# Kernel tuning notes

Hardware: AMD Instinct MI355X
Metric: run time of the kernel (lower is better)

The kernel has to match this reference:

```python
import jax, jax.numpy as jnp
import numpy as np

N = 1_000_000
MU_PRIOR = 0.6447


def setup_inputs() -> dict:
    key = jax.random.key(0)
    ks = jax.random.split(key, 8)
    pred_ = jax.random.normal(ks[0], (N, 9), jnp.float32)
    Y_obs = jax.random.normal(ks[1], (N, 9), jnp.float32)
    rrs = jax.random.normal(ks[2], (N, 5), jnp.float32)
    rrs_pred = jax.random.normal(ks[3], (N, 5), jnp.float32)
    nan_array = jax.random.normal(ks[4], (N, 9), jnp.float32)  # all finite -> lens = 9
    # cov_z must be SPD so log(det(cov_z)) is finite
    A = jax.random.normal(ks[5], (N, 3, 3), jnp.float32) * 0.3
    cov_z = jnp.einsum('nij,nkj->nik', A, A) + 0.5 * jnp.eye(3, dtype=jnp.float32)
    mu_z = jax.random.normal(ks[6], (N, 3), jnp.float32)
    parameters = 1.0 + 0.01 * jax.random.normal(ks[7], (64,), jnp.float32)
    return {"pred_": pred_, "Y_obs": Y_obs, "rrs": rrs, "rrs_pred": rrs_pred,
            "nan_array": nan_array, "cov_z": cov_z, "mu_z": mu_z,
            "parameters": parameters}


def reference(pred_, Y_obs, rrs, rrs_pred, nan_array, cov_z, mu_z, parameters):
    n = pred_.shape[0]
    # --- buffers built in __init__ (default multipliers = ones) ---
    se_diag = jnp.asarray([0.0015, 0.0012, 0.001, 0.00086, 0.00057], jnp.float32) ** 2
    rrs_cov_inv = jnp.linalg.inv(jnp.diag(se_diag))            # [5,5]
    Y_cov_inv = jnp.eye(9, dtype=jnp.float32)                  # [9,9]
    s_a = jnp.eye(3, dtype=jnp.float32) * 4.9                  # [3,3]
    s_a_inv = jnp.linalg.inv(s_a)                              # [3,3]

    # trace((X) @ Cinv @ X.T) == sum_n x_n^T Cinv x_n  (trace trick, O(N))
    dr = rrs - rrs_pred                                        # [N,5]
    rrs_error = jnp.einsum('ni,ij,nj->', dr, rrs_cov_inv, dr) / (5.0 * n)

    lens = jnp.sum(~jnp.isnan(nan_array), axis=1).astype(jnp.float32)  # [N]
    dy = pred_ - Y_obs                                         # [N,9]
    obs_quad = jnp.einsum('ni,ij,nj->n', dy, Y_cov_inv, dy)    # [N]
    obs_error = jnp.sum(obs_quad / lens) / n

    # KL(N(mu_z, cov_z) || N(0.6447, s_a)) style term
    logdet_sa = jnp.log(jnp.linalg.det(s_a))
    logdet_cz = jnp.log(jnp.linalg.det(cov_z))                 # [N]
    tr_term = jnp.einsum('ij,nji->n', s_a_inv, cov_z)          # trace(s_a_inv @ cov_z)
    dm = mu_z - MU_PRIOR                                       # [N,3]
    DK = 0.5 * jnp.sum(logdet_sa - logdet_cz + tr_term) / n \
         + 0.5 * jnp.einsum('ni,ij,nj->', dm, s_a_inv, dm) / (3.0 * n)

    l2_norm = jnp.mean((parameters - 1.0) ** 2)
    return rrs_error + 10.0 * obs_error + DK + l2_norm
```

## Files before the change

### kernel.cpp

```cpp
#include <hip/hip_runtime.h>
#include <math.h>

#define MU_PRIOR   0.6447f
#define LOGDET_SA  4.767705615349743f
#define INV_SA     (1.0f/4.9f)

#define CW      64
#define NF4C    144
#define NF4R    80
#define NF4M    48
#define GRID    2048

#define W0 (1.0f / (0.0015f  * 0.0015f))
#define W1 (1.0f / (0.0012f  * 0.0012f))
#define W2 (1.0f / (0.0010f  * 0.0010f))
#define W3 (1.0f / (0.00086f * 0.00086f))
#define W4 (1.0f / (0.00057f * 0.00057f))

__device__ __forceinline__ float warp_reduce_f(float v) {
#pragma unroll
    for (int off = 32; off > 0; off >>= 1) v += __shfl_down(v, off, 64);
    return v;
}

__device__ __forceinline__ double warp_reduce_d(double v) {
#pragma unroll
    for (int off = 32; off > 0; off >>= 1) v += __shfl_down(v, off, 64);
    return v;
}

__device__ __forceinline__ float comb1(float p, float y, float n) {
    const float d = p - y;
    const float d2 = d * d;
    const unsigned u = __float_as_uint(d2) | ((n == n) ? 0u : 0x80000000u);
    return __uint_as_float(u);
}
__device__ __forceinline__ float4 comb4(float4 p, float4 y, float4 n) {
    float4 o;
    o.x = comb1(p.x, y.x, n.x); o.y = comb1(p.y, y.y, n.y);
    o.z = comb1(p.z, y.z, n.z); o.w = comb1(p.w, y.w, n.w);
    return o;
}

__global__ __launch_bounds__(256) void loss_main(
    const float* __restrict__ pred, const float* __restrict__ yobs,
    const float* __restrict__ rrs,  const float* __restrict__ rrsp,
    const float* __restrict__ nanarr, const float* __restrict__ cov,
    const float* __restrict__ mu, double* __restrict__ partial, int nchunks)
{
    __shared__ float4 sV[4 * NF4C];
    __shared__ float4 sC[4 * NF4C];

    const int tid  = threadIdx.x;
    const int lane = tid & 63;
    const int wid  = tid >> 6;
    const int wslot = wid * NF4C;
    const int wgid  = blockIdx.x * 4 + wid;
    const int nw    = (int)gridDim.x * 4;

    const int w0 = (5 - (lane % 5)) % 5;
    float ew[5];
#pragma unroll
    for (int k = 0; k < 5; ++k) {
        int idx = w0 + k; if (idx >= 5) idx -= 5;
        ew[k] = (idx == 0) ? W0 : (idx == 1) ? W1 : (idx == 2) ? W2
               : (idx == 3) ? W3 : W4;
    }

    float acc = 0.0f;

    for (int c = wgid; c < nchunks; c += nw) {
        const float4* gP = reinterpret_cast<const float4*>(pred)   + (size_t)c * NF4C;
        const float4* gY = reinterpret_cast<const float4*>(yobs)   + (size_t)c * NF4C;
        const float4* gN = reinterpret_cast<const float4*>(nanarr) + (size_t)c * NF4C;
        const float4* gC = reinterpret_cast<const float4*>(cov)    + (size_t)c * NF4C;
        const float4* gR = reinterpret_cast<const float4*>(rrs)    + (size_t)c * NF4R;
        const float4* gQ = reinterpret_cast<const float4*>(rrsp)   + (size_t)c * NF4R;
        const float4* gM = reinterpret_cast<const float4*>(mu)     + (size_t)c * NF4M;

        const float4 p0 = gP[lane], p1 = gP[lane + 64];
        const float4 y0 = gY[lane], y1 = gY[lane + 64];
        const float4 n0 = gN[lane], n1 = gN[lane + 64];
        const float4 c0 = gC[lane], c1 = gC[lane + 64];
        const float4 r0 = gR[lane], q0 = gQ[lane];
        float4 p2, y2, n2, c2, r1, q1, m0;
        if (lane < 16) {
            p2 = gP[lane + 128]; y2 = gY[lane + 128];
            n2 = gN[lane + 128]; c2 = gC[lane + 128];
            r1 = gR[lane + 64];  q1 = gQ[lane + 64];
        }
        if (lane < 48) m0 = gM[lane];

        {
            float ra = 0.f;
            const float d0 = r0.x - q0.x, d1 = r0.y - q0.y;
            const float d2 = r0.z - q0.z, d3 = r0.w - q0.w;
            ra += d0 * d0 * ew[0] + d1 * d1 * ew[1]
                + d2 * d2 * ew[2] + d3 * d3 * ew[3];
            if (lane < 16) {
                const float e0 = r1.x - q1.x, e1 = r1.y - q1.y;
                const float e2 = r1.z - q1.z, e3 = r1.w - q1.w;
                ra += e0 * e0 * ew[1] + e1 * e1 * ew[2]
                    + e2 * e2 * ew[3] + e3 * e3 * ew[4];
            }
            acc += ra * 0.2f;
        }

        if (lane < 48) {
            const float d0 = m0.x - MU_PRIOR, d1 = m0.y - MU_PRIOR;
            const float d2 = m0.z - MU_PRIOR, d3 = m0.w - MU_PRIOR;
            acc += (d0 * d0 + d1 * d1 + d2 * d2 + d3 * d3) * (1.0f / 29.4f);
        }

        sV[wslot + lane]       = comb4(p0, y0, n0);
        sV[wslot + lane + 64]  = comb4(p1, y1, n1);
        sC[wslot + lane]       = c0;
        sC[wslot + lane + 64]  = c1;
        if (lane < 16) {
            sV[wslot + lane + 128] = comb4(p2, y2, n2);
            sC[wslot + lane + 128] = c2;
        }

        __builtin_amdgcn_wave_barrier();

        {
            const float* v = reinterpret_cast<const float*>(sV + wslot) + 9 * lane;
            const float* m = reinterpret_cast<const float*>(sC + wslot) + 9 * lane;
            float dy2 = 0.f, len = 0.f;
#pragma unroll
            for (int k = 0; k < 9; ++k) {
                const unsigned u = __float_as_uint(v[k]);
                dy2 += __uint_as_float(u & 0x7fffffffu);
                len += (float)(1u - (u >> 31));
            }
            acc += 10.0f * dy2 / len;

            const float tr  = m[0] + m[4] + m[8];
            const float det = m[0] * (m[4] * m[8] - m[5] * m[7])
                            - m[1] * (m[3] * m[8] - m[5] * m[6])
                            + m[2] * (m[3] * m[7] - m[4] * m[6]);
            acc += 0.5f * (LOGDET_SA - __logf(det) + tr * INV_SA);
        }

        __builtin_amdgcn_wave_barrier();
    }

    acc = warp_reduce_f(acc);
    __shared__ float smem[4];
    if (lane == 0) smem[wid] = acc;
    __syncthreads();
    if (tid == 0)
        partial[blockIdx.x] = (double)(smem[0] + smem[1] + smem[2] + smem[3]);
}

__global__ __launch_bounds__(256) void loss_final(
    const double* __restrict__ partial, int npartials,
    const float* __restrict__ params, int nparams,
    const float* __restrict__ pred, const float* __restrict__ yobs,
    const float* __restrict__ rrs,  const float* __restrict__ rrsp,
    const float* __restrict__ nanarr, const float* __restrict__ cov,
    const float* __restrict__ mu, int mainRows, int rows,
    float* __restrict__ out)
{
    double accA = 0.0;
    double accB = 0.0;

    for (int i = threadIdx.x; i < npartials; i += 256) accA += partial[i];
    for (int i = threadIdx.x; i < nparams; i += 256) {
        const float d = params[i] - 1.0f;
        accB += (double)(d * d);
    }

    for (int r = mainRows + (int)threadIdx.x; r < rows; r += 256) {
        float dy2 = 0.f, len = 0.f;
        for (int i = 0; i < 9; ++i) {
            const float d = pred[9 * (size_t)r + i] - yobs[9 * (size_t)r + i];
            dy2 += d * d;
            const float v = nanarr[9 * (size_t)r + i];
            len += (v == v) ? 1.f : 0.f;
        }
        const float W[5] = {W0, W1, W2, W3, W4};
        float racc = 0.f;
        for (int i = 0; i < 5; ++i) {
            const float d = rrs[5 * (size_t)r + i] - rrsp[5 * (size_t)r + i];
            racc += d * d * W[i];
        }
        const float* m = cov + 9 * (size_t)r;
        const float tr  = m[0] + m[4] + m[8];
        const float det = m[0] * (m[4] * m[8] - m[5] * m[7])
                        - m[1] * (m[3] * m[8] - m[5] * m[6])
                        + m[2] * (m[3] * m[7] - m[4] * m[6]);
        float dm = 0.f;
        for (int i = 0; i < 3; ++i) {
            const float d = mu[3 * (size_t)r + i] - MU_PRIOR;
            dm += d * d;
        }
        accA += (double)(racc * 0.2f + 10.f * dy2 / len
                         + 0.5f * (LOGDET_SA - __logf(det) + tr * INV_SA)
                         + dm * (1.f / 29.4f));
    }

    double val = accA * (1.0 / (double)rows) + accB * (1.0 / (double)nparams);
    val = warp_reduce_d(val);
    __shared__ double sm[4];
    const int lane = threadIdx.x & 63;
    const int wid  = threadIdx.x >> 6;
    if (lane == 0) sm[wid] = val;
    __syncthreads();
    if (threadIdx.x == 0)
        out[0] = (float)(sm[0] + sm[1] + sm[2] + sm[3]);
}

extern "C" void kernel_launch(void* const* d_in, const int* in_sizes, int n_in,
                              void* d_out, int out_size, void* d_ws, size_t ws_size,
                              hipStream_t stream) {
    const float* pred   = (const float*)d_in[0];
    const float* yobs   = (const float*)d_in[1];
    const float* rrs    = (const float*)d_in[2];
    const float* rrsp   = (const float*)d_in[3];
    const float* nanarr = (const float*)d_in[4];
    const float* cov    = (const float*)d_in[5];
    const float* mu     = (const float*)d_in[6];
    const float* params = (const float*)d_in[7];
    float* out = (float*)d_out;

    const int rows     = in_sizes[0] / 9;
    const int nchunks  = rows / CW;
    const int mainRows = nchunks * CW;
    int grid = (nchunks * 4 < GRID * 4) ? ((nchunks + 3) / 4 > 0 ? (nchunks + 3) / 4 : 1) : GRID;
    if (grid > GRID) grid = GRID;

    double* partial = (double*)d_ws;

    loss_main<<<grid, 256, 0, stream>>>(pred, yobs, rrs, rrsp, nanarr,
                                        cov, mu, partial, nchunks);
    loss_final<<<1, 256, 0, stream>>>(partial, grid, params, in_sizes[7],
                                      pred, yobs, rrs, rrsp, nanarr, cov, mu,
                                      mainRows, rows, out);
}
```

Before: 208.1 us.

## Fuse final reduction into main kernel and double-buffer chunk loads per wave

The separate final-reduction kernel is replaced by a last-block-done pattern, using an atomic counter reset by a memset before launch. Each wave now issues global loads for two chunks before computing either, to raise memory-level parallelism. The grid is sized so each wave handles pairs of chunks. This costs higher register pressure, which could lower occupancy, plus an extra memset operation and atomic traffic.

```diff
diff --git a/kernel.cpp b/kernel.cpp
--- a/kernel.cpp
+++ b/kernel.cpp
@@ -42,18 +42,117 @@
     return o;
 }
 
-__global__ __launch_bounds__(256) void loss_main(
+struct ChunkRegs {
+    float4 p0, p1, p2, y0, y1, y2, n0, n1, n2, c0, c1, c2;
+    float4 r0, q0, r1, q1, m0;
+};
+
+__device__ __forceinline__ void issue_loads(
+    ChunkRegs& R, int c, int lane,
     const float* __restrict__ pred, const float* __restrict__ yobs,
     const float* __restrict__ rrs,  const float* __restrict__ rrsp,
     const float* __restrict__ nanarr, const float* __restrict__ cov,
-    const float* __restrict__ mu, double* __restrict__ partial, int nchunks)
+    const float* __restrict__ mu)
+{
+    const float4* gP = reinterpret_cast<const float4*>(pred)   + (size_t)c * NF4C;
+    const float4* gY = reinterpret_cast<const float4*>(yobs)   + (size_t)c * NF4C;
+    const float4* gN = reinterpret_cast<const float4*>(nanarr) + (size_t)c * NF4C;
+    const float4* gC = reinterpret_cast<const float4*>(cov)    + (size_t)c * NF4C;
+    const float4* gR = reinterpret_cast<const float4*>(rrs)    + (size_t)c * NF4R;
+    const float4* gQ = reinterpret_cast<const float4*>(rrsp)   + (size_t)c * NF4R;
+    const float4* gM = reinterpret_cast<const float4*>(mu)     + (size_t)c * NF4M;
+
+    R.p0 = gP[lane]; R.p1 = gP[lane + 64];
+    R.y0 = gY[lane]; R.y1 = gY[lane + 64];
+    R.n0 = gN[lane]; R.n1 = gN[lane + 64];
+    R.c0 = gC[lane]; R.c1 = gC[lane + 64];
+    R.r0 = gR[lane]; R.q0 = gQ[lane];
+    if (lane < 16) {
+        R.p2 = gP[lane + 128]; R.y2 = gY[lane + 128];
+        R.n2 = gN[lane + 128]; R.c2 = gC[lane + 128];
+        R.r1 = gR[lane + 64];  R.q1 = gQ[lane + 64];
+    }
+    if (lane < 48) R.m0 = gM[lane];
+}
+
+__device__ __forceinline__ float compute_chunk(
+    const ChunkRegs& R, float4* __restrict__ sVw, float4* __restrict__ sCw,
+    int lane, const float ew[5])
+{
+    float acc = 0.0f;
+
+    {
+        float ra = 0.f;
+        const float d0 = R.r0.x - R.q0.x, d1 = R.r0.y - R.q0.y;
+        const float d2 = R.r0.z - R.q0.z, d3 = R.r0.w - R.q0.w;
+        ra += d0 * d0 * ew[0] + d1 * d1 * ew[1]
+            + d2 * d2 * ew[2] + d3 * d3 * ew[3];
+        if (lane < 16) {
+            const float e0 = R.r1.x - R.q1.x, e1 = R.r1.y - R.q1.y;
+            const float e2 = R.r1.z - R.q1.z, e3 = R.r1.w - R.q1.w;
+            ra += e0 * e0 * ew[1] + e1 * e1 * ew[2]
+                + e2 * e2 * ew[3] + e3 * e3 * ew[4];
+        }
+        acc += ra * 0.2f;
+    }
+
+    if (lane < 48) {
+        const float d0 = R.m0.x - MU_PRIOR, d1 = R.m0.y - MU_PRIOR;
+        const float d2 = R.m0.z - MU_PRIOR, d3 = R.m0.w - MU_PRIOR;
+        acc += (d0 * d0 + d1 * d1 + d2 * d2 + d3 * d3) * (1.0f / 29.4f);
+    }
+
+    sVw[lane]       = comb4(R.p0, R.y0, R.n0);
+    sVw[lane + 64]  = comb4(R.p1, R.y1, R.n1);
+    sCw[lane]       = R.c0;
+    sCw[lane + 64]  = R.c1;
+    if (lane < 16) {
+        sVw[lane + 128] = comb4(R.p2, R.y2, R.n2);
+        sCw[lane + 128] = R.c2;
+    }
+
+    __builtin_amdgcn_wave_barrier();
+
+    {
+        const float* v = reinterpret_cast<const float*>(sVw) + 9 * lane;
+        const float* m = reinterpret_cast<const float*>(sCw) + 9 * lane;
+        float dy2 = 0.f, len = 0.f;
+#pragma unroll
+        for (int k = 0; k < 9; ++k) {
+            const unsigned u = __float_as_uint(v[k]);
+            dy2 += __uint_as_float(u & 0x7fffffffu);
+            len += (float)(1u - (u >> 31));
+        }
+        acc += 10.0f * dy2 / len;
+
+        const float tr  = m[0] + m[4] + m[8];
+        const float det = m[0] * (m[4] * m[8] - m[5] * m[7])
+                        - m[1] * (m[3] * m[8] - m[5] * m[6])
+                        + m[2] * (m[3] * m[7] - m[4] * m[6]);
+        acc += 0.5f * (LOGDET_SA - __logf(det) + tr * INV_SA);
+    }
+
+    __builtin_amdgcn_wave_barrier();
+    return acc;
+}
+
+__global__ __launch_bounds__(256) void loss_fused(
+    const float* __restrict__ pred, const float* __restrict__ yobs,
+    const float* __restrict__ rrs,  const float* __restrict__ rrsp,
+    const float* __restrict__ nanarr, const float* __restrict__ cov,
+    const float* __restrict__ mu, const float* __restrict__ params,
+    double* __restrict__ partial, unsigned* __restrict__ counter,
+    int nchunks, int rows, int nparams, float* __restrict__ out)
 {
     __shared__ float4 sV[4 * NF4C];
     __shared__ float4 sC[4 * NF4C];
-
-    const int tid  = threadIdx.x;
-    const int lane = tid & 63;
-    const int wid  = tid >> 6;
+    __shared__ float  smem[4];
+    __shared__ double smd[4];
+    __shared__ int    amLast;
+
+    const int tid   = threadIdx.x;
+    const int lane  = tid & 63;
+    const int wid   = tid >> 6;
     const int wslot = wid * NF4C;
     const int wgid  = blockIdx.x * 4 + wid;
     const int nw    = (int)gridDim.x * 4;
@@ -69,109 +168,45 @@
 
     float acc = 0.0f;
 
-    for (int c = wgid; c < nchunks; c += nw) {
-        const float4* gP = reinterpret_cast<const float4*>(pred)   + (size_t)c * NF4C;
-        const float4* gY = reinterpret_cast<const float4*>(yobs)   + (size_t)c * NF4C;
-        const float4* gN = reinterpret_cast<const float4*>(nanarr) + (size_t)c * NF4C;
-        const float4* gC = reinterpret_cast<const float4*>(cov)    + (size_t)c * NF4C;
-        const float4* gR = reinterpret_cast<const float4*>(rrs)    + (size_t)c * NF4R;
-        const float4* gQ = reinterpret_cast<const float4*>(rrsp)   + (size_t)c * NF4R;
-        const float4* gM = reinterpret_cast<const float4*>(mu)     + (size_t)c * NF4M;
-
-        const float4 p0 = gP[lane], p1 = gP[lane + 64];
-        const float4 y0 = gY[lane], y1 = gY[lane + 64];
-        const float4 n0 = gN[lane], n1 = gN[lane + 64];
-        const float4 c0 = gC[lane], c1 = gC[lane + 64];
-        const float4 r0 = gR[lane], q0 = gQ[lane];
-        float4 p2, y2, n2, c2, r1, q1, m0;
-        if (lane < 16) {
-            p2 = gP[lane + 128]; y2 = gY[lane + 128];
-            n2 = gN[lane + 128]; c2 = gC[lane + 128];
-            r1 = gR[lane + 64];  q1 = gQ[lane + 64];
-        }
-        if (lane < 48) m0 = gM[lane];
-
-        {
-            float ra = 0.f;
-            const float d0 = r0.x - q0.x, d1 = r0.y - q0.y;
-            const float d2 = r0.z - q0.z, d3 = r0.w - q0.w;
-            ra += d0 * d0 * ew[0] + d1 * d1 * ew[1]
-                + d2 * d2 * ew[2] + d3 * d3 * ew[3];
-            if (lane < 16) {
-                const float e0 = r1.x - q1.x, e1 = r1.y - q1.y;
-                const float e2 = r1.z - q1.z, e3 = r1.w - q1.w;
-                ra += e0 * e0 * ew[1] + e1 * e1 * ew[2]
-                    + e2 * e2 * ew[3] + e3 * e3 * ew[4];
-            }
-            acc += ra * 0.2f;
-        }
-
-        if (lane < 48) {
-            const float d0 = m0.x - MU_PRIOR, d1 = m0.y - MU_PRIOR;
-            const float d2 = m0.z - MU_PRIOR, d3 = m0.w - MU_PRIOR;
-            acc += (d0 * d0 + d1 * d1 + d2 * d2 + d3 * d3) * (1.0f / 29.4f);
-        }
-
-        sV[wslot + lane]       = comb4(p0, y0, n0);
-        sV[wslot + lane + 64]  = comb4(p1, y1, n1);
-        sC[wslot + lane]       = c0;
-        sC[wslot + lane + 64]  = c1;
-        if (lane < 16) {
-            sV[wslot + lane + 128] = comb4(p2, y2, n2);
-            sC[wslot + lane + 128] = c2;
-        }
-
-        __builtin_amdgcn_wave_barrier();
-
-        {
-            const float* v = reinterpret_cast<const float*>(sV + wslot) + 9 * lane;
-            const float* m = reinterpret_cast<const float*>(sC + wslot) + 9 * lane;
-            float dy2 = 0.f, len = 0.f;
-#pragma unroll
-            for (int k = 0; k < 9; ++k) {
-                const unsigned u = __float_as_uint(v[k]);
-                dy2 += __uint_as_float(u & 0x7fffffffu);
-                len += (float)(1u - (u >> 31));
-            }
-            acc += 10.0f * dy2 / len;
-
-            const float tr  = m[0] + m[4] + m[8];
-            const float det = m[0] * (m[4] * m[8] - m[5] * m[7])
-                            - m[1] * (m[3] * m[8] - m[5] * m[6])
-                            + m[2] * (m[3] * m[7] - m[4] * m[6]);
-            acc += 0.5f * (LOGDET_SA - __logf(det) + tr * INV_SA);
-        }
-
-        __builtin_amdgcn_wave_barrier();
+    for (int c0 = 2 * wgid; c0 < nchunks; c0 += 2 * nw) {
+        const int  c1   = c0 + 1;
+        const bool hasB = (c1 < nchunks);
+        ChunkRegs A, B;
+        issue_loads(A, c0, lane, pred, yobs, rrs, rrsp, nanarr, cov, mu);
+        if (hasB)
+            issue_loads(B, c1, lane, pred, yobs, rrs, rrsp, nanarr, cov, mu);
+        acc += compute_chunk(A, sV + wslot, sC + wslot, lane, ew);
+        if (hasB)
+            acc += compute_chunk(B, sV + wslot, sC + wslot, lane, ew);
     }
 
     acc = warp_reduce_f(acc);
-    __shared__ float smem[4];
     if (lane == 0) smem[wid] = acc;
     __syncthreads();
-    if (tid == 0)
-        partial[blockIdx.x] = (double)(smem[0] + smem[1] + smem[2] + smem[3]);
-}
-
-__global__ __launch_bounds__(256) void loss_final(
-    const double* __restrict__ partial, int npartials,
-    const float* __restrict__ params, int nparams,
-    const float* __restrict__ pred, const float* __restrict__ yobs,
-    const float* __restrict__ rrs,  const float* __restrict__ rrsp,
-    const float* __restrict__ nanarr, const float* __restrict__ cov,
-    const float* __restrict__ mu, int mainRows, int rows,
-    float* __restrict__ out)
-{
+    if (tid == 0) {
+        const double bsum = (double)(smem[0] + smem[1] + smem[2] + smem[3]);
+        __hip_atomic_store(&partial[blockIdx.x], bsum,
+                           __ATOMIC_RELEASE, __HIP_MEMORY_SCOPE_AGENT);
+        const unsigned prev = __hip_atomic_fetch_add(
+            counter, 1u, __ATOMIC_ACQ_REL, __HIP_MEMORY_SCOPE_AGENT);
+        amLast = (prev == (unsigned)gridDim.x - 1u);
+    }
+    __syncthreads();
+    if (!amLast) return;
+
     double accA = 0.0;
     double accB = 0.0;
 
-    for (int i = threadIdx.x; i < npartials; i += 256) accA += partial[i];
-    for (int i = threadIdx.x; i < nparams; i += 256) {
+    for (int i = tid; i < (int)gridDim.x; i += 256)
+        accA += __hip_atomic_load(&partial[i],
+                                  __ATOMIC_RELAXED, __HIP_MEMORY_SCOPE_AGENT);
+    for (int i = tid; i < nparams; i += 256) {
         const float d = params[i] - 1.0f;
         accB += (double)(d * d);
     }
 
-    for (int r = mainRows + (int)threadIdx.x; r < rows; r += 256) {
+    const int mainRows = nchunks * CW;
+    for (int r = mainRows + tid; r < rows; r += 256) {
         float dy2 = 0.f, len = 0.f;
         for (int i = 0; i < 9; ++i) {
             const float d = pred[9 * (size_t)r + i] - yobs[9 * (size_t)r + i];
@@ -202,13 +237,10 @@
 
     double val = accA * (1.0 / (double)rows) + accB * (1.0 / (double)nparams);
     val = warp_reduce_d(val);
-    __shared__ double sm[4];
-    const int lane = threadIdx.x & 63;
-    const int wid  = threadIdx.x >> 6;
-    if (lane == 0) sm[wid] = val;
+    if (lane == 0) smd[wid] = val;
     __syncthreads();
-    if (threadIdx.x == 0)
-        out[0] = (float)(sm[0] + sm[1] + sm[2] + sm[3]);
+    if (tid == 0)
+        out[0] = (float)(smd[0] + smd[1] + smd[2] + smd[3]);
 }
 
 extern "C" void kernel_launch(void* const* d_in, const int* in_sizes, int n_in,
@@ -224,17 +256,18 @@
     const float* params = (const float*)d_in[7];
     float* out = (float*)d_out;
 
-    const int rows     = in_sizes[0] / 9;
-    const int nchunks  = rows / CW;
-    const int mainRows = nchunks * CW;
-    int grid = (nchunks * 4 < GRID * 4) ? ((nchunks + 3) / 4 > 0 ? (nchunks + 3) / 4 : 1) : GRID;
+    const int rows    = in_sizes[0] / 9;
+    const int nchunks = rows / CW;
+
+    int grid = (nchunks + 7) / 8;
+    if (grid < 1) grid = 1;
     if (grid > GRID) grid = GRID;
 
-    double* partial = (double*)d_ws;
-
-    loss_main<<<grid, 256, 0, stream>>>(pred, yobs, rrs, rrsp, nanarr,
-                                        cov, mu, partial, nchunks);
-    loss_final<<<1, 256, 0, stream>>>(partial, grid, params, in_sizes[7],
-                                      pred, yobs, rrs, rrsp, nanarr, cov, mu,
-                                      mainRows, rows, out);
-}
+    double*   partial = (double*)d_ws;
+    unsigned* counter = (unsigned*)((char*)d_ws + (size_t)GRID * sizeof(double));
+
+    hipMemsetAsync(counter, 0, sizeof(unsigned), stream);
+    loss_fused<<<grid, 256, 0, stream>>>(pred, yobs, rrs, rrsp, nanarr,
+                                         cov, mu, params, partial, counter,
+                                         nchunks, rows, in_sizes[7], out);
+}
```

New measurement: 376.0 us. 80.7% more time.

## Double-buffer chunk staging with direct global-to-LDS loads

Applied to the files above, without the earlier changes.

Replaces the register-staged loads of pred, Y_obs, nan_array and cov_z with global_load_lds, which writes those chunks straight into LDS. Each wave alternates between two buffers, loading the next chunk while it computes on the current one, so memory latency can overlap with compute. The grid drops from 2048 to 512 blocks to make room for the larger LDS footprint, which limits resident waves per CU. Correctness depends on the compiler inserting the right memory waits around the asynchronous LDS writes.

```diff
diff --git a/kernel.cpp b/kernel.cpp
--- a/kernel.cpp
+++ b/kernel.cpp
@@ -9,7 +9,13 @@
 #define NF4C    144
 #define NF4R    80
 #define NF4M    48
-#define GRID    2048
+#define GRID    512
+
+#define BUF_P   0
+#define BUF_Y   2304
+#define BUF_N   4608
+#define BUF_C   6912
+#define BUFSZ   9216
 
 #define W0 (1.0f / (0.0015f  * 0.0015f))
 #define W1 (1.0f / (0.0012f  * 0.0012f))
@@ -29,17 +35,93 @@
     return v;
 }
 
-__device__ __forceinline__ float comb1(float p, float y, float n) {
-    const float d = p - y;
-    const float d2 = d * d;
-    const unsigned u = __float_as_uint(d2) | ((n == n) ? 0u : 0x80000000u);
-    return __uint_as_float(u);
-}
-__device__ __forceinline__ float4 comb4(float4 p, float4 y, float4 n) {
-    float4 o;
-    o.x = comb1(p.x, y.x, n.x); o.y = comb1(p.y, y.y, n.y);
-    o.z = comb1(p.z, y.z, n.z); o.w = comb1(p.w, y.w, n.w);
-    return o;
+__device__ __forceinline__ void gld16(const void* g, void* l) {
+    __builtin_amdgcn_global_load_lds(g, l, 16, 0, 0);
+}
+
+__device__ __forceinline__ void stage_chunk(
+    char* lb, int c, int lane,
+    const float* __restrict__ pred, const float* __restrict__ yobs,
+    const float* __restrict__ nanarr, const float* __restrict__ cov)
+{
+    const float4* gP = reinterpret_cast<const float4*>(pred)   + (size_t)c * NF4C + lane;
+    const float4* gY = reinterpret_cast<const float4*>(yobs)   + (size_t)c * NF4C + lane;
+    const float4* gN = reinterpret_cast<const float4*>(nanarr) + (size_t)c * NF4C + lane;
+    const float4* gC = reinterpret_cast<const float4*>(cov)    + (size_t)c * NF4C + lane;
+    gld16(gP,      lb + BUF_P);
+    gld16(gP + 64, lb + BUF_P + 1024);
+    gld16(gY,      lb + BUF_Y);
+    gld16(gY + 64, lb + BUF_Y + 1024);
+    gld16(gN,      lb + BUF_N);
+    gld16(gN + 64, lb + BUF_N + 1024);
+    gld16(gC,      lb + BUF_C);
+    gld16(gC + 64, lb + BUF_C + 1024);
+    if (lane < 16) {
+        gld16(gP + 128, lb + BUF_P + 2048);
+        gld16(gY + 128, lb + BUF_Y + 2048);
+        gld16(gN + 128, lb + BUF_N + 2048);
+        gld16(gC + 128, lb + BUF_C + 2048);
+    }
+}
+
+__device__ __forceinline__ float body(
+    const char* lb, int c, int lane, const float ew[5],
+    const float* __restrict__ rrs, const float* __restrict__ rrsp,
+    const float* __restrict__ mu)
+{
+    const float4* gR = reinterpret_cast<const float4*>(rrs)  + (size_t)c * NF4R;
+    const float4* gQ = reinterpret_cast<const float4*>(rrsp) + (size_t)c * NF4R;
+    const float4* gM = reinterpret_cast<const float4*>(mu)   + (size_t)c * NF4M;
+    const float4 r0 = gR[lane], q0 = gQ[lane];
+    float4 r1, q1, m0;
+    if (lane < 16) { r1 = gR[lane + 64]; q1 = gQ[lane + 64]; }
+    if (lane < 48) m0 = gM[lane];
+
+    float acc = 0.0f;
+
+    {
+        const float* P = reinterpret_cast<const float*>(lb + BUF_P) + 9 * lane;
+        const float* Y = reinterpret_cast<const float*>(lb + BUF_Y) + 9 * lane;
+        const float* A = reinterpret_cast<const float*>(lb + BUF_N) + 9 * lane;
+        const float* M = reinterpret_cast<const float*>(lb + BUF_C) + 9 * lane;
+        float dy2 = 0.f, len = 0.f;
+#pragma unroll
+        for (int k = 0; k < 9; ++k) {
+            const float d = P[k] - Y[k];
+            dy2 += d * d;
+            const float nv = A[k];
+            len += (nv == nv) ? 1.f : 0.f;
+        }
+        acc += 10.0f * dy2 / len;
+
+        const float tr  = M[0] + M[4] + M[8];
+        const float det = M[0] * (M[4] * M[8] - M[5] * M[7])
+                        - M[1] * (M[3] * M[8] - M[5] * M[6])
+                        + M[2] * (M[3] * M[7] - M[4] * M[6]);
+        acc += 0.5f * (LOGDET_SA - __logf(det) + tr * INV_SA);
+    }
+
+    {
+        float ra = 0.f;
+        const float d0 = r0.x - q0.x, d1 = r0.y - q0.y;
+        const float d2 = r0.z - q0.z, d3 = r0.w - q0.w;
+        ra += d0 * d0 * ew[0] + d1 * d1 * ew[1]
+            + d2 * d2 * ew[2] + d3 * d3 * ew[3];
+        if (lane < 16) {
+            const float e0 = r1.x - q1.x, e1 = r1.y - q1.y;
+            const float e2 = r1.z - q1.z, e3 = r1.w - q1.w;
+            ra += e0 * e0 * ew[1] + e1 * e1 * ew[2]
+                + e2 * e2 * ew[3] + e3 * e3 * ew[4];
+        }
+        acc += ra * 0.2f;
+    }
+
+    if (lane < 48) {
+        const float d0 = m0.x - MU_PRIOR, d1 = m0.y - MU_PRIOR;
+        const float d2 = m0.z - MU_PRIOR, d3 = m0.w - MU_PRIOR;
+        acc += (d0 * d0 + d1 * d1 + d2 * d2 + d3 * d3) * (1.0f / 29.4f);
+    }
+    return acc;
 }
 
 __global__ __launch_bounds__(256) void loss_main(
@@ -48,15 +130,18 @@
     const float* __restrict__ nanarr, const float* __restrict__ cov,
     const float* __restrict__ mu, double* __restrict__ partial, int nchunks)
 {
-    __shared__ float4 sV[4 * NF4C];
-    __shared__ float4 sC[4 * NF4C];
+    __shared__ __align__(16) char sA[4][BUFSZ];
+    __shared__ __align__(16) char sB[4][BUFSZ];
+    __shared__ float smem[4];
 
     const int tid  = threadIdx.x;
     const int lane = tid & 63;
     const int wid  = tid >> 6;
-    const int wslot = wid * NF4C;
-    const int wgid  = blockIdx.x * 4 + wid;
-    const int nw    = (int)gridDim.x * 4;
+    const int wgid = blockIdx.x * 4 + wid;
+    const int nw   = (int)gridDim.x * 4;
+
+    char* bufA = sA[wid];
+    char* bufB = sB[wid];
 
     const int w0 = (5 - (lane % 5)) % 5;
     float ew[5];
@@ -69,84 +154,24 @@
 
     float acc = 0.0f;
 
-    for (int c = wgid; c < nchunks; c += nw) {
-        const float4* gP = reinterpret_cast<const float4*>(pred)   + (size_t)c * NF4C;
-        const float4* gY = reinterpret_cast<const float4*>(yobs)   + (size_t)c * NF4C;
-        const float4* gN = reinterpret_cast<const float4*>(nanarr) + (size_t)c * NF4C;
-        const float4* gC = reinterpret_cast<const float4*>(cov)    + (size_t)c * NF4C;
-        const float4* gR = reinterpret_cast<const float4*>(rrs)    + (size_t)c * NF4R;
-        const float4* gQ = reinterpret_cast<const float4*>(rrsp)   + (size_t)c * NF4R;
-        const float4* gM = reinterpret_cast<const float4*>(mu)     + (size_t)c * NF4M;
-
-        const float4 p0 = gP[lane], p1 = gP[lane + 64];
-        const float4 y0 = gY[lane], y1 = gY[lane + 64];
-        const float4 n0 = gN[lane], n1 = gN[lane + 64];
-        const float4 c0 = gC[lane], c1 = gC[lane + 64];
-        const float4 r0 = gR[lane], q0 = gQ[lane];
-        float4 p2, y2, n2, c2, r1, q1, m0;
-        if (lane < 16) {
-            p2 = gP[lane + 128]; y2 = gY[lane + 128];
-            n2 = gN[lane + 128]; c2 = gC[lane + 128];
-            r1 = gR[lane + 64];  q1 = gQ[lane + 64];
-        }
-        if (lane < 48) m0 = gM[lane];
-
-        {
-            float ra = 0.f;
-            const float d0 = r0.x - q0.x, d1 = r0.y - q0.y;
-            const float d2 = r0.z - q0.z, d3 = r0.w - q0.w;
-            ra += d0 * d0 * ew[0] + d1 * d1 * ew[1]
-                + d2 * d2 * ew[2] + d3 * d3 * ew[3];
-            if (lane < 16) {
-                const float e0 = r1.x - q1.x, e1 = r1.y - q1.y;
-                const float e2 = r1.z - q1.z, e3 = r1.w - q1.w;
-                ra += e0 * e0 * ew[1] + e1 * e1 * ew[2]
-                    + e2 * e2 * ew[3] + e3 * e3 * ew[4];
-            }
-            acc += ra * 0.2f;
-        }
-
-        if (lane < 48) {
-            const float d0 = m0.x - MU_PRIOR, d1 = m0.y - MU_PRIOR;
-            const float d2 = m0.z - MU_PRIOR, d3 = m0.w - MU_PRIOR;
-            acc += (d0 * d0 + d1 * d1 + d2 * d2 + d3 * d3) * (1.0f / 29.4f);
-        }
-
-        sV[wslot + lane]       = comb4(p0, y0, n0);
-        sV[wslot + lane + 64]  = comb4(p1, y1, n1);
-        sC[wslot + lane]       = c0;
-        sC[wslot + lane + 64]  = c1;
-        if (lane < 16) {
-            sV[wslot + lane + 128] = comb4(p2, y2, n2);
-            sC[wslot + lane + 128] = c2;
-        }
-
-        __builtin_amdgcn_wave_barrier();
-
-        {
-            const float* v = reinterpret_cast<const float*>(sV + wslot) + 9 * lane;
-            const float* m = reinterpret_cast<const float*>(sC + wslot) + 9 * lane;
-            float dy2 = 0.f, len = 0.f;
-#pragma unroll
-            for (int k = 0; k < 9; ++k) {
-                const unsigned u = __float_as_uint(v[k]);
-                dy2 += __uint_as_float(u & 0x7fffffffu);
-                len += (float)(1u - (u >> 31));
-            }
-            acc += 10.0f * dy2 / len;
-
-            const float tr  = m[0] + m[4] + m[8];
-            const float det = m[0] * (m[4] * m[8] - m[5] * m[7])
-                            - m[1] * (m[3] * m[8] - m[5] * m[6])
-                            + m[2] * (m[3] * m[7] - m[4] * m[6]);
-            acc += 0.5f * (LOGDET_SA - __logf(det) + tr * INV_SA);
-        }
-
-        __builtin_amdgcn_wave_barrier();
+    if (wgid < nchunks)
+        stage_chunk(bufA, wgid, lane, pred, yobs, nanarr, cov);
+
+    int c = wgid;
+    while (c < nchunks) {
+        if (c + nw < nchunks)
+            stage_chunk(bufB, c + nw, lane, pred, yobs, nanarr, cov);
+        acc += body(bufA, c, lane, ew, rrs, rrsp, mu);
+        c += nw;
+        if (c >= nchunks) break;
+
+        if (c + nw < nchunks)
+            stage_chunk(bufA, c + nw, lane, pred, yobs, nanarr, cov);
+        acc += body(bufB, c, lane, ew, rrs, rrsp, mu);
+        c += nw;
     }
 
     acc = warp_reduce_f(acc);
-    __shared__ float smem[4];
     if (lane == 0) smem[wid] = acc;
     __syncthreads();
     if (tid == 0)
@@ -227,7 +252,8 @@
     const int rows     = in_sizes[0] / 9;
     const int nchunks  = rows / CW;
     const int mainRows = nchunks * CW;
-    int grid = (nchunks * 4 < GRID * 4) ? ((nchunks + 3) / 4 > 0 ? (nchunks + 3) / 4 : 1) : GRID;
+    int grid = (nchunks + 3) / 4;
+    if (grid < 1) grid = 1;
     if (grid > GRID) grid = GRID;
 
     double* partial = (double*)d_ws;
```

Measured after the change: 206.6 us. About the same (-0.7%).

## Replace LDS-staged chunked loads with direct per-row unaligned vector loads

Applied to the files above, without the earlier changes.

Drops the per-wave 64-row chunk scheme, which used coalesced float4 loads staged through shared memory, and has each thread read its own row directly with 4-byte-aligned vector loads, running a grid-stride loop unrolled by two. This removes the LDS traffic, the wave barriers and the tail-row handling in the final kernel, and halves the grid size. In exchange, global loads become strided per thread (36-byte row stride) and less coalesced, which may use DRAM bandwidth less efficiently.

```diff
diff --git a/kernel.cpp b/kernel.cpp
--- a/kernel.cpp
+++ b/kernel.cpp
@@ -5,17 +5,18 @@
 #define LOGDET_SA  4.767705615349743f
 #define INV_SA     (1.0f/4.9f)
 
-#define CW      64
-#define NF4C    144
-#define NF4R    80
-#define NF4M    48
-#define GRID    2048
+#define GRID    1024
 
 #define W0 (1.0f / (0.0015f  * 0.0015f))
 #define W1 (1.0f / (0.0012f  * 0.0012f))
 #define W2 (1.0f / (0.0010f  * 0.0010f))
 #define W3 (1.0f / (0.00086f * 0.00086f))
 #define W4 (1.0f / (0.00057f * 0.00057f))
+
+typedef float f4_t __attribute__((ext_vector_type(4)));
+typedef f4_t uf4 __attribute__((aligned(4)));
+typedef float f2_t __attribute__((ext_vector_type(2)));
+typedef f2_t uf2 __attribute__((aligned(4)));
 
 __device__ __forceinline__ float warp_reduce_f(float v) {
 #pragma unroll
@@ -29,138 +30,93 @@
     return v;
 }
 
-__device__ __forceinline__ float comb1(float p, float y, float n) {
-    const float d = p - y;
-    const float d2 = d * d;
-    const unsigned u = __float_as_uint(d2) | ((n == n) ? 0u : 0x80000000u);
-    return __uint_as_float(u);
-}
-__device__ __forceinline__ float4 comb4(float4 p, float4 y, float4 n) {
-    float4 o;
-    o.x = comb1(p.x, y.x, n.x); o.y = comb1(p.y, y.y, n.y);
-    o.z = comb1(p.z, y.z, n.z); o.w = comb1(p.w, y.w, n.w);
-    return o;
-}
-
 __global__ __launch_bounds__(256) void loss_main(
     const float* __restrict__ pred, const float* __restrict__ yobs,
     const float* __restrict__ rrs,  const float* __restrict__ rrsp,
     const float* __restrict__ nanarr, const float* __restrict__ cov,
-    const float* __restrict__ mu, double* __restrict__ partial, int nchunks)
+    const float* __restrict__ mu, double* __restrict__ partial, int rows)
 {
-    __shared__ float4 sV[4 * NF4C];
-    __shared__ float4 sC[4 * NF4C];
-
-    const int tid  = threadIdx.x;
-    const int lane = tid & 63;
-    const int wid  = tid >> 6;
-    const int wslot = wid * NF4C;
-    const int wgid  = blockIdx.x * 4 + wid;
-    const int nw    = (int)gridDim.x * 4;
-
-    const int w0 = (5 - (lane % 5)) % 5;
-    float ew[5];
-#pragma unroll
-    for (int k = 0; k < 5; ++k) {
-        int idx = w0 + k; if (idx >= 5) idx -= 5;
-        ew[k] = (idx == 0) ? W0 : (idx == 1) ? W1 : (idx == 2) ? W2
-               : (idx == 3) ? W3 : W4;
-    }
+    const int tid    = blockIdx.x * 256 + threadIdx.x;
+    const int stride = (int)gridDim.x * 256;
 
     float acc = 0.0f;
 
-    for (int c = wgid; c < nchunks; c += nw) {
-        const float4* gP = reinterpret_cast<const float4*>(pred)   + (size_t)c * NF4C;
-        const float4* gY = reinterpret_cast<const float4*>(yobs)   + (size_t)c * NF4C;
-        const float4* gN = reinterpret_cast<const float4*>(nanarr) + (size_t)c * NF4C;
-        const float4* gC = reinterpret_cast<const float4*>(cov)    + (size_t)c * NF4C;
-        const float4* gR = reinterpret_cast<const float4*>(rrs)    + (size_t)c * NF4R;
-        const float4* gQ = reinterpret_cast<const float4*>(rrsp)   + (size_t)c * NF4R;
-        const float4* gM = reinterpret_cast<const float4*>(mu)     + (size_t)c * NF4M;
+#pragma unroll 2
+    for (int r = tid; r < rows; r += stride) {
+        const float* P = pred   + 9 * (size_t)r;
+        const float* Y = yobs   + 9 * (size_t)r;
+        const float* A = nanarr + 9 * (size_t)r;
+        const float* C = cov    + 9 * (size_t)r;
+        const float* R = rrs    + 5 * (size_t)r;
+        const float* Q = rrsp   + 5 * (size_t)r;
+        const float* M = mu     + 3 * (size_t)r;
 
-        const float4 p0 = gP[lane], p1 = gP[lane + 64];
-        const float4 y0 = gY[lane], y1 = gY[lane + 64];
-        const float4 n0 = gN[lane], n1 = gN[lane + 64];
-        const float4 c0 = gC[lane], c1 = gC[lane + 64];
-        const float4 r0 = gR[lane], q0 = gQ[lane];
-        float4 p2, y2, n2, c2, r1, q1, m0;
-        if (lane < 16) {
-            p2 = gP[lane + 128]; y2 = gY[lane + 128];
-            n2 = gN[lane + 128]; c2 = gC[lane + 128];
-            r1 = gR[lane + 64];  q1 = gQ[lane + 64];
+        const uf4 p0 = *(const uf4*)P;       const uf4 p1 = *(const uf4*)(P + 4);
+        const float p8 = P[8];
+        const uf4 y0 = *(const uf4*)Y;       const uf4 y1 = *(const uf4*)(Y + 4);
+        const float y8 = Y[8];
+        const uf4 a0 = *(const uf4*)A;       const uf4 a1 = *(const uf4*)(A + 4);
+        const float a8 = A[8];
+        const uf4 c0 = *(const uf4*)C;       const uf4 c1 = *(const uf4*)(C + 4);
+        const float c8 = C[8];
+        const uf4 r0 = *(const uf4*)R;       const float r4 = R[4];
+        const uf4 q0 = *(const uf4*)Q;       const float q4 = Q[4];
+        const uf2 m0 = *(const uf2*)M;       const float m2 = M[2];
+
+        float dy2, len;
+        {
+            const float d0 = p0.x - y0.x, d1 = p0.y - y0.y;
+            const float d2 = p0.z - y0.z, d3 = p0.w - y0.w;
+            const float d4 = p1.x - y1.x, d5 = p1.y - y1.y;
+            const float d6 = p1.z - y1.z, d7 = p1.w - y1.w;
+            const float d8 = p8 - y8;
+            dy2 = d0*d0 + d1*d1 + d2*d2 + d3*d3 + d4*d4
+                + d5*d5 + d6*d6 + d7*d7 + d8*d8;
+            len = ((a0.x == a0.x) ? 1.f : 0.f) + ((a0.y == a0.y) ? 1.f : 0.f)
+                + ((a0.z == a0.z) ? 1.f : 0.f) + ((a0.w == a0.w) ? 1.f : 0.f)
+                + ((a1.x == a1.x) ? 1.f : 0.f) + ((a1.y == a1.y) ? 1.f : 0.f)
+                + ((a1.z == a1.z) ? 1.f : 0.f) + ((a1.w == a1.w) ? 1.f : 0.f)
+                + ((a8   == a8  ) ? 1.f : 0.f);
         }
-        if (lane < 48) m0 = gM[lane];
+        acc += 10.0f * dy2 / len;
 
         {
-            float ra = 0.f;
-            const float d0 = r0.x - q0.x, d1 = r0.y - q0.y;
-            const float d2 = r0.z - q0.z, d3 = r0.w - q0.w;
-            ra += d0 * d0 * ew[0] + d1 * d1 * ew[1]
-                + d2 * d2 * ew[2] + d3 * d3 * ew[3];
-            if (lane < 16) {
-                const float e0 = r1.x - q1.x, e1 = r1.y - q1.y;
-                const float e2 = r1.z - q1.z, e3 = r1.w - q1.w;
-                ra += e0 * e0 * ew[1] + e1 * e1 * ew[2]
-                    + e2 * e2 * ew[3] + e3 * e3 * ew[4];
-            }
-            acc += ra * 0.2f;
-        }
-
-        if (lane < 48) {
-            const float d0 = m0.x - MU_PRIOR, d1 = m0.y - MU_PRIOR;
-            const float d2 = m0.z - MU_PRIOR, d3 = m0.w - MU_PRIOR;
-            acc += (d0 * d0 + d1 * d1 + d2 * d2 + d3 * d3) * (1.0f / 29.4f);
-        }
-
-        sV[wslot + lane]       = comb4(p0, y0, n0);
-        sV[wslot + lane + 64]  = comb4(p1, y1, n1);
-        sC[wslot + lane]       = c0;
-        sC[wslot + lane + 64]  = c1;
-        if (lane < 16) {
-            sV[wslot + lane + 128] = comb4(p2, y2, n2);
-            sC[wslot + lane + 128] = c2;
-        }
-
-        __builtin_amdgcn_wave_barrier();
-
-        {
-            const float* v = reinterpret_cast<const float*>(sV + wslot) + 9 * lane;
-            const float* m = reinterpret_cast<const float*>(sC + wslot) + 9 * lane;
-            float dy2 = 0.f, len = 0.f;
-#pragma unroll
-            for (int k = 0; k < 9; ++k) {
-                const unsigned u = __float_as_uint(v[k]);
-                dy2 += __uint_as_float(u & 0x7fffffffu);
-                len += (float)(1u - (u >> 31));
-            }
-            acc += 10.0f * dy2 / len;
-
-            const float tr  = m[0] + m[4] + m[8];
-            const float det = m[0] * (m[4] * m[8] - m[5] * m[7])
-                            - m[1] * (m[3] * m[8] - m[5] * m[6])
-                            + m[2] * (m[3] * m[7] - m[4] * m[6]);
+            const float tr  = c0.x + c1.x + c8;
+            const float det = c0.x * (c1.x * c8   - c1.y * c1.w)
+                            - c0.y * (c0.w * c8   - c1.y * c1.z)
+                            + c0.z * (c0.w * c1.w - c1.x * c1.z);
             acc += 0.5f * (LOGDET_SA - __logf(det) + tr * INV_SA);
         }
 
-        __builtin_amdgcn_wave_barrier();
+        {
+            const float d0 = r0.x - q0.x, d1 = r0.y - q0.y;
+            const float d2 = r0.z - q0.z, d3 = r0.w - q0.w;
+            const float d4 = r4 - q4;
+            acc += (d0*d0*W0 + d1*d1*W1 + d2*d2*W2 + d3*d3*W3 + d4*d4*W4)
+                   * 0.2f;
+        }
+
+        {
+            const float d0 = m0.x - MU_PRIOR, d1 = m0.y - MU_PRIOR;
+            const float d2 = m2 - MU_PRIOR;
+            acc += (d0*d0 + d1*d1 + d2*d2) * (1.0f / 29.4f);
+        }
     }
 
     acc = warp_reduce_f(acc);
     __shared__ float smem[4];
+    const int lane = threadIdx.x & 63;
+    const int wid  = threadIdx.x >> 6;
     if (lane == 0) smem[wid] = acc;
     __syncthreads();
-    if (tid == 0)
+    if (threadIdx.x == 0)
         partial[blockIdx.x] = (double)(smem[0] + smem[1] + smem[2] + smem[3]);
 }
 
 __global__ __launch_bounds__(256) void loss_final(
     const double* __restrict__ partial, int npartials,
     const float* __restrict__ params, int nparams,
-    const float* __restrict__ pred, const float* __restrict__ yobs,
-    const float* __restrict__ rrs,  const float* __restrict__ rrsp,
-    const float* __restrict__ nanarr, const float* __restrict__ cov,
-    const float* __restrict__ mu, int mainRows, int rows,
-    float* __restrict__ out)
+    int rows, float* __restrict__ out)
 {
     double accA = 0.0;
     double accB = 0.0;
@@ -169,35 +125,6 @@
     for (int i = threadIdx.x; i < nparams; i += 256) {
         const float d = params[i] - 1.0f;
         accB += (double)(d * d);
-    }
-
-    for (int r = mainRows + (int)threadIdx.x; r < rows; r += 256) {
-        float dy2 = 0.f, len = 0.f;
-        for (int i = 0; i < 9; ++i) {
-            const float d = pred[9 * (size_t)r + i] - yobs[9 * (size_t)r + i];
-            dy2 += d * d;
-            const float v = nanarr[9 * (size_t)r + i];
-            len += (v == v) ? 1.f : 0.f;
-        }
-        const float W[5] = {W0, W1, W2, W3, W4};
-        float racc = 0.f;
-        for (int i = 0; i < 5; ++i) {
-            const float d = rrs[5 * (size_t)r + i] - rrsp[5 * (size_t)r + i];
-            racc += d * d * W[i];
-        }
-        const float* m = cov + 9 * (size_t)r;
-        const float tr  = m[0] + m[4] + m[8];
-        const float det = m[0] * (m[4] * m[8] - m[5] * m[7])
-                        - m[1] * (m[3] * m[8] - m[5] * m[6])
-                        + m[2] * (m[3] * m[7] - m[4] * m[6]);
-        float dm = 0.f;
-        for (int i = 0; i < 3; ++i) {
-            const float d = mu[3 * (size_t)r + i] - MU_PRIOR;
-            dm += d * d;
-        }
-        accA += (double)(racc * 0.2f + 10.f * dy2 / len
-                         + 0.5f * (LOGDET_SA - __logf(det) + tr * INV_SA)
-                         + dm * (1.f / 29.4f));
     }
 
     double val = accA * (1.0 / (double)rows) + accB * (1.0 / (double)nparams);
@@ -224,17 +151,16 @@
     const float* params = (const float*)d_in[7];
     float* out = (float*)d_out;
 
-    const int rows     = in_sizes[0] / 9;
-    const int nchunks  = rows / CW;
-    const int mainRows = nchunks * CW;
-    int grid = (nchunks * 4 < GRID * 4) ? ((nchunks + 3) / 4 > 0 ? (nchunks + 3) / 4 : 1) : GRID;
+    const int rows = in_sizes[0] / 9;
+
+    int grid = (rows + 255) / 256;
     if (grid > GRID) grid = GRID;
+    if (grid < 1) grid = 1;
 
     double* partial = (double*)d_ws;
 
     loss_main<<<grid, 256, 0, stream>>>(pred, yobs, rrs, rrsp, nanarr,
-                                        cov, mu, partial, nchunks);
+                                        cov, mu, partial, rows);
     loss_final<<<1, 256, 0, stream>>>(partial, grid, params, in_sizes[7],
-                                      pred, yobs, rrs, rrsp, nanarr, cov, mu,
-                                      mainRows, rows, out);
+                                      rows, out);
 }
```

Result: no change. 206.7 us (-0.6%).
